# Performance work log

Measured on AMD Instinct MI355X. Metric: run time of the kernel, lower is better.

## Reference

```python
import jax, jax.numpy as jnp
import numpy as np

B, N, H = 2, 1024, 768
MAX_W = 30
WIDTH_D = 20
SPAN_DIM = 3 * H + WIDTH_D  # 2324
K = int(N * 0.4)  # 409 (eval mode: // (1+0) )


def _enumerate_spans(n, max_w):
    # Replicates: enumerate_spans then sorted(spans[::-1], key=start)
    # -> start ascending, end DESCENDING within each start.
    spans = []
    for s in range(n):
        for e in range(min(s + max_w - 1, n - 1), s - 1, -1):
            spans.append((s, e))
    return np.asarray(spans, dtype=np.int32)  # [num_spans, 2]


def setup_inputs() -> dict:
    key = jax.random.key(0)
    ks = jax.random.split(key, 8)
    spans = jnp.asarray(_enumerate_spans(N, MAX_W))  # [30285, 2]
    return {
        "segment_embeddings": jax.random.normal(ks[0], (B, N, H), jnp.float32),
        "segment_mask": jnp.ones((B, N), jnp.int32),
        "candidate_spans": spans,
        "width_emb": jax.random.normal(ks[1], (MAX_W, WIDTH_D), jnp.float32) * 0.02,
        "W1": jax.random.normal(ks[2], (SPAN_DIM, H), jnp.float32) * 0.02,
        "b1": jax.random.normal(ks[3], (H,), jnp.float32) * 0.02,
        "w_s": jax.random.normal(ks[4], (H,), jnp.float32) * 0.02,
        "b_s": jax.random.normal(ks[5], (1,), jnp.float32) * 0.02,
        "k": K,
    }


def reference(segment_embeddings, segment_mask, candidate_spans, width_emb, W1, b1, w_s, b_s, k):
    starts = candidate_spans[:, 0]  # [S]
    ends = candidate_spans[:, 1]    # [S]
    # Endpoint span extractor: x, y, x*y + width embedding (width = end-start)
    x = segment_embeddings[:, starts, :]          # [B,S,H]
    y = segment_embeddings[:, ends, :]            # [B,S,H]
    wemb = width_emb[ends - starts]               # [S,WIDTH_D]
    bsz = segment_embeddings.shape[0]
    span_feat = jnp.concatenate(
        [x, y, x * y, jnp.broadcast_to(wemb[None], (bsz,) + wemb.shape)], axis=-1
    )  # [B,S,3H+WD]
    # MLP (dropout is identity in eval) + GELU (torch default: exact erf)
    h = jax.nn.gelu(jnp.einsum("bsd,dh->bsh", span_feat, W1) + b1, approximate=False)
    scores = jnp.einsum("bsh,h->bs", h, w_s) + b_s[0]  # [B,S]
    # Mask spans whose end index exceeds valid length
    lengths = segment_mask.sum(-1)  # [B]
    scores = scores + jnp.where(ends[None, :] >= lengths[:, None], -1e6, 0.0)
    # Top-k prune, then sort indices and gather
    _, idx = jax.lax.top_k(scores, k)          # [B,k]
    idx = jnp.sort(idx, axis=1)
    top_scores = jnp.take_along_axis(scores, idx, axis=1)            # [B,k]
    top_span_embs = jnp.take_along_axis(h, idx[:, :, None], axis=1)  # [B,k,H]
    top_spans = candidate_spans[idx]                                 # [B,k,2]
    return top_span_embs, top_scores, top_spans
```

## Files before the change

kernel.cpp:

```cpp
#include <hip/hip_runtime.h>
#include <math.h>

#define NB 2
#define NN 1024
#define HH 768
#define MAXW 30
#define KTOP 409
#define BANDCAP 4096
#define BAND_TAU 2e-2f
#define FILTCAP 6144
#define CHT 120
#define GROWS 512

typedef __attribute__((ext_vector_type(4))) float f32x4;
typedef __attribute__((ext_vector_type(8))) __bf16 bf16x8;
typedef __attribute__((ext_vector_type(8))) unsigned short us8;

__device__ __forceinline__ float gelu_f(float z) {
  return 0.5f * z * (1.0f + erff(z * 0.70710678118654752440f));
}
__device__ __forceinline__ unsigned f2key(float f) {
  unsigned u = __float_as_uint(f);
  return (u & 0x80000000u) ? ~u : (u | 0x80000000u);
}
__device__ __forceinline__ float key2f(unsigned k) {
  unsigned u = (k & 0x80000000u) ? (k & 0x7fffffffu) : ~k;
  return __uint_as_float(u);
}
__device__ __forceinline__ unsigned short f2bf_rn(float f) {
  unsigned u = __float_as_uint(f);
  unsigned r = u + 0x7fffu + ((u >> 16) & 1u);
  return (unsigned short)(r >> 16);
}
__device__ __forceinline__ float bf2f(unsigned short h) {
  return __uint_as_float(((unsigned)h) << 16);
}
__device__ __forceinline__ void async_copy16(const void* g, void* l) {
  __builtin_amdgcn_global_load_lds(
      (const __attribute__((address_space(1))) unsigned int*)g,
      (__attribute__((address_space(3))) unsigned int*)l, 16, 0, 0);
}

__global__ void len_kernel(const int* __restrict__ mask, int* __restrict__ lengths) {
  __shared__ int red[256];
  for (int b = 0; b < NB; ++b) {
    int s = 0;
    for (int i = threadIdx.x; i < NN; i += 256) s += mask[b * NN + i];
    red[threadIdx.x] = s;
    __syncthreads();
    for (int off = 128; off > 0; off >>= 1) {
      if (threadIdx.x < off) red[threadIdx.x] += red[threadIdx.x + off];
      __syncthreads();
    }
    if (threadIdx.x == 0) lengths[b] = red[0];
    __syncthreads();
  }
}

__global__ void r_kernel(const float* __restrict__ wemb, const float* __restrict__ W1,
                         const float* __restrict__ b1, float* __restrict__ R) {
  int w = blockIdx.x;
  for (int h = threadIdx.x; h < HH; h += 256) {
    float acc = b1[h];
    for (int j = 0; j < 20; ++j)
      acc = fmaf(wemb[w * 20 + j], W1[(size_t)(3 * HH + j) * HH + h], acc);
    R[w * HH + h] = acc;
  }
}

__global__ __launch_bounds__(256) void prep_bt_kernel(const float* __restrict__ W1,
                                                      unsigned short* __restrict__ Bt,
                                                      unsigned short* __restrict__ Btlo) {
  const int ki = blockIdx.x;
  const int hby = blockIdx.y;
  const float* W1c = W1 + (size_t)(2 * HH) * HH;
  const int t = threadIdx.x;
#pragma unroll
  for (int half = 0; half < 2; ++half) {
    const int c = t + half * 256;
    const int col = c >> 2, kg = c & 3;
    us8 hv, lv;
#pragma unroll
    for (int j = 0; j < 8; ++j) {
      const int k = ki * 32 + kg * 8 + j;
      float v = W1c[(size_t)k * HH + hby * 128 + col];
      unsigned short h = f2bf_rn(v);
      hv[j] = h;
      lv[j] = f2bf_rn(v - bf2f(h));
    }
    const size_t bo = ((size_t)(hby * 24 + ki) * 512 + c) * 8;
    *(us8*)(Bt + bo) = hv;
    *(us8*)(Btlo + bo) = lv;
  }
}

__global__ __launch_bounds__(256) void prep_emb_hl_kernel(
    const float* __restrict__ emb, unsigned short* __restrict__ Ahi,
    unsigned short* __restrict__ Alo) {
  const int tile = blockIdx.x;
  const int ki = blockIdx.y;
  const int t = threadIdx.x;
#pragma unroll
  for (int half = 0; half < 2; ++half) {
    const int c = t + half * 256;
    const int row = c >> 2, kgs = c & 3;
    const int kg = kgs ^ ((row >> 1) & 3);
    const float* xr = emb + (size_t)(tile * 128 + row) * HH;
    const int k0 = ki * 32 + kg * 8;
    float4 x0 = *(const float4*)(xr + k0);
    float4 x1 = *(const float4*)(xr + k0 + 4);
    const float xv[8] = {x0.x, x0.y, x0.z, x0.w, x1.x, x1.y, x1.z, x1.w};
    us8 hv, lv;
#pragma unroll
    for (int j = 0; j < 8; ++j) {
      unsigned short h = f2bf_rn(xv[j]);
      hv[j] = h;
      lv[j] = f2bf_rn(xv[j] - bf2f(h));
    }
    const size_t base = (((size_t)tile * 24 + ki) * 512 + c) * 8;
    *(us8*)(Ahi + base) = hv;
    *(us8*)(Alo + base) = lv;
  }
}

__global__ __launch_bounds__(256) void prep_w1ab_kernel(
    const float* __restrict__ W1, unsigned short* __restrict__ Bhi,
    unsigned short* __restrict__ Blo) {
  const int ki = blockIdx.x;
  const int hby = blockIdx.y;
  const int t = threadIdx.x;
#pragma unroll
  for (int half = 0; half < 2; ++half) {
    const int c = t + half * 256;
    const int col = c >> 2, kg = c & 3;
    const int gc = hby * 128 + col;
    const float* base = W1 + (gc < 768 ? (size_t)0 : (size_t)HH * HH);
    const int n = (gc < 768) ? gc : gc - 768;
    us8 hv, lv;
#pragma unroll
    for (int j = 0; j < 8; ++j) {
      const int k = ki * 32 + kg * 8 + j;
      float v = base[(size_t)k * HH + n];
      unsigned short h = f2bf_rn(v);
      hv[j] = h;
      lv[j] = f2bf_rn(v - bf2f(h));
    }
    const size_t bo = (((size_t)hby * 24 + ki) * 512 + c) * 8;
    *(us8*)(Bhi + bo) = hv;
    *(us8*)(Blo + bo) = lv;
  }
}

__global__ __launch_bounds__(256) void pq_mfma_kernel(
    const unsigned short* __restrict__ Ahi, const unsigned short* __restrict__ Alo,
    const unsigned short* __restrict__ Bhi, const unsigned short* __restrict__ Blo,
    float* __restrict__ P, float* __restrict__ Q) {
  __shared__ unsigned short AsmH[128 * 32], AsmL[128 * 32];
  const int tile = blockIdx.x;
  const int hby = blockIdx.y;
  const int tid = threadIdx.x;
  const int lane = tid & 63, w = tid >> 6;
  const int wm = w & 1, wn = w >> 1;
  const int lm = lane & 15, lq = lane >> 4;

  f32x4 acc[4][4];
#pragma unroll
  for (int i = 0; i < 4; ++i)
#pragma unroll
    for (int j = 0; j < 4; ++j) acc[i][j] = (f32x4){0.f, 0.f, 0.f, 0.f};

  const unsigned short* AbH = Ahi + (size_t)tile * 24 * 4096;
  const unsigned short* AbL = Alo + (size_t)tile * 24 * 4096;
  const unsigned short* BbH = Bhi + (size_t)hby * 24 * 4096;
  const unsigned short* BbL = Blo + (size_t)hby * 24 * 4096;
  const int a_off = (wm * 64 + lm) * 32 + (lq ^ ((lm >> 1) & 3)) * 8;
  const int b_off = (wn * 64 + lm) * 32 + lq * 8;

  for (int ki = 0; ki < 24; ++ki) {
    async_copy16(AbH + (size_t)ki * 4096 + tid * 8, AsmH + tid * 8);
    async_copy16(AbH + (size_t)ki * 4096 + (tid + 256) * 8, AsmH + (tid + 256) * 8);
    async_copy16(AbL + (size_t)ki * 4096 + tid * 8, AsmL + tid * 8);
    async_copy16(AbL + (size_t)ki * 4096 + (tid + 256) * 8, AsmL + (tid + 256) * 8);
    bf16x8 bh[4], bl[4];
#pragma unroll
    for (int ni = 0; ni < 4; ++ni) {
      bh[ni] = *reinterpret_cast<const bf16x8*>(BbH + (size_t)ki * 4096 + b_off + ni * 512);
      bl[ni] = *reinterpret_cast<const bf16x8*>(BbL + (size_t)ki * 4096 + b_off + ni * 512);
    }
    __syncthreads();
    bf16x8 ah[4], al[4];
#pragma unroll
    for (int mi = 0; mi < 4; ++mi) {
      ah[mi] = *reinterpret_cast<const bf16x8*>(AsmH + a_off + mi * 512);
      al[mi] = *reinterpret_cast<const bf16x8*>(AsmL + a_off + mi * 512);
    }
#pragma unroll
    for (int ni = 0; ni < 4; ++ni)
#pragma unroll
      for (int mi = 0; mi < 4; ++mi) {
        acc[mi][ni] = __builtin_amdgcn_mfma_f32_16x16x32_bf16(ah[mi], bh[ni], acc[mi][ni], 0, 0, 0);
        acc[mi][ni] = __builtin_amdgcn_mfma_f32_16x16x32_bf16(ah[mi], bl[ni], acc[mi][ni], 0, 0, 0);
        acc[mi][ni] = __builtin_amdgcn_mfma_f32_16x16x32_bf16(al[mi], bh[ni], acc[mi][ni], 0, 0, 0);
      }
    __syncthreads();
  }

  float* Obase = (hby < 6) ? P : Q;
  const int cb = ((hby < 6) ? hby : hby - 6) * 128 + wn * 64 + lm;
  const int rowb = tile * 128 + wm * 64 + lq * 4;
#pragma unroll
  for (int mi = 0; mi < 4; ++mi)
#pragma unroll
    for (int ni = 0; ni < 4; ++ni)
#pragma unroll
      for (int r = 0; r < 4; ++r)
        Obase[(size_t)(rowb + mi * 16 + r) * HH + cb + ni * 16] = acc[mi][ni][r];
}

__global__ __launch_bounds__(256) void prep_a_kernel(
    const float* __restrict__ emb, const int* __restrict__ spans,
    unsigned short* __restrict__ At, int S, int tileofs) {
  const int tl = blockIdx.x, b = blockIdx.y;
  const int tile = tileofs + tl;
  const int t = threadIdx.x;
#pragma unroll
  for (int half = 0; half < 2; ++half) {
    const int c = t + half * 256;
    const int row = c >> 2, kgs = c & 3;
    const int kg = kgs ^ ((row >> 1) & 3);
    int g = tile * 128 + row;
    if (g >= S) g = S - 1;
    const int s = spans[2 * g], e = spans[2 * g + 1];
    const float* xr = emb + ((size_t)b * NN + s) * HH;
    const float* yr = emb + ((size_t)b * NN + e) * HH;
    unsigned short* dst = At + (((size_t)b * CHT + tl) * 24 * 512 + c) * 8;
    for (int ki = 0; ki < 24; ++ki) {
      const int k0 = ki * 32 + kg * 8;
      float4 x0 = *(const float4*)(xr + k0);
      float4 x1 = *(const float4*)(xr + k0 + 4);
      float4 y0 = *(const float4*)(yr + k0);
      float4 y1 = *(const float4*)(yr + k0 + 4);
      us8 v;
      v[0] = f2bf_rn(x0.x * y0.x); v[1] = f2bf_rn(x0.y * y0.y);
      v[2] = f2bf_rn(x0.z * y0.z); v[3] = f2bf_rn(x0.w * y0.w);
      v[4] = f2bf_rn(x1.x * y1.x); v[5] = f2bf_rn(x1.y * y1.y);
      v[6] = f2bf_rn(x1.z * y1.z); v[7] = f2bf_rn(x1.w * y1.w);
      *(us8*)(dst + (size_t)ki * 4096) = v;
    }
  }
}

__global__ __launch_bounds__(256, 3) void score_mfma3_kernel(
    const int* __restrict__ spans,
    const unsigned short* __restrict__ At, const unsigned short* __restrict__ Bt,
    const float* __restrict__ w_s,
    const float* __restrict__ P, const float* __restrict__ Q, const float* __restrict__ R,
    float* __restrict__ spart, int S, int tileofs) {
  __shared__ unsigned short Asm[128 * 32];
  __shared__ int ssm[128], eem[128], wwm[128];
  __shared__ float sred[128 * 2];

  const int hby = blockIdx.x;
  const int tl = blockIdx.y;
  const int tile = tileofs + tl;
  const int b = blockIdx.z;
  const int tid = threadIdx.x;
  const int lane = tid & 63, w = tid >> 6;
  const int wm = w & 1, wn = w >> 1;
  const int lm = lane & 15, lq = lane >> 4;

  if (tid < 128) {
    int g = tile * 128 + tid;
    int gg = g < S ? g : S - 1;
    int s = spans[2 * gg], e = spans[2 * gg + 1];
    ssm[tid] = s; eem[tid] = e; wwm[tid] = e - s;
  }

  f32x4 acc[4][4];
#pragma unroll
  for (int i = 0; i < 4; ++i)
#pragma unroll
    for (int j = 0; j < 4; ++j) acc[i][j] = (f32x4){0.f, 0.f, 0.f, 0.f};

  const unsigned short* Ab = At + ((size_t)b * CHT + tl) * 24 * 4096;
  const unsigned short* Bb = Bt + (size_t)hby * 24 * 4096;
  const int a_off = (wm * 64 + lm) * 32 + (lq ^ ((lm >> 1) & 3)) * 8;
  const int b_off = (wn * 64 + lm) * 32 + lq * 8;

  for (int ki = 0; ki < 24; ++ki) {
    async_copy16(Ab + (size_t)ki * 4096 + tid * 8, Asm + tid * 8);
    async_copy16(Ab + (size_t)ki * 4096 + (tid + 256) * 8, Asm + (tid + 256) * 8);
    bf16x8 bfr[4];
#pragma unroll
    for (int ni = 0; ni < 4; ++ni)
      bfr[ni] = *reinterpret_cast<const bf16x8*>(Bb + (size_t)ki * 4096 + b_off + ni * 512);
    __syncthreads();
    bf16x8 afr[4];
#pragma unroll
    for (int mi = 0; mi < 4; ++mi)
      afr[mi] = *reinterpret_cast<const bf16x8*>(Asm + a_off + mi * 512);
#pragma unroll
    for (int ni = 0; ni < 4; ++ni)
#pragma unroll
      for (int mi = 0; mi < 4; ++mi)
        acc[mi][ni] = __builtin_amdgcn_mfma_f32_16x16x32_bf16(afr[mi], bfr[ni], acc[mi][ni], 0, 0, 0);
    __syncthreads();
  }

  const int hbg = hby * 128;
  float wsv[4];
#pragma unroll
  for (int ni = 0; ni < 4; ++ni) wsv[ni] = w_s[hbg + wn * 64 + ni * 16 + lm];

#pragma unroll
  for (int mi = 0; mi < 4; ++mi) {
#pragma unroll
    for (int r = 0; r < 4; ++r) {
      const int rowl = wm * 64 + mi * 16 + lq * 4 + r;
      const int s = ssm[rowl], e = eem[rowl], wd = wwm[rowl];
      const float* Pp = P + ((size_t)b * NN + s) * HH + hbg + wn * 64 + lm;
      const float* Qp = Q + ((size_t)b * NN + e) * HH + hbg + wn * 64 + lm;
      const float* Rp = R + (size_t)wd * HH + hbg + wn * 64 + lm;
      float psum = 0.f;
#pragma unroll
      for (int ni = 0; ni < 4; ++ni) {
        float z = acc[mi][ni][r] + Pp[ni * 16] + Qp[ni * 16] + Rp[ni * 16];
        psum = fmaf(gelu_f(z), wsv[ni], psum);
      }
      psum += __shfl_xor(psum, 1);
      psum += __shfl_xor(psum, 2);
      psum += __shfl_xor(psum, 4);
      psum += __shfl_xor(psum, 8);
      if (lm == 0) sred[rowl * 2 + wn] = psum;
    }
  }
  __syncthreads();
  if (tid < 128) {
    int g = tile * 128 + tid;
    if (g < S)
      spart[(size_t)hby * ((size_t)NB * S) + (size_t)b * S + g] = sred[tid * 2] + sred[tid * 2 + 1];
  }
}

__global__ void combine_kernel(const float* __restrict__ sp, const int* __restrict__ spans,
                               const float* __restrict__ b_s, const int* __restrict__ lengths,
                               float* __restrict__ scores, int S) {
  int idx = blockIdx.x * 256 + threadIdx.x;
  if (idx >= NB * S) return;
  int b = idx / S, i = idx - b * S;
  size_t st = (size_t)NB * S;
  float v = b_s[0];
#pragma unroll
  for (int j = 0; j < 6; ++j) v += sp[j * st + idx];
  if (spans[2 * i + 1] >= lengths[b]) v += -1000000.0f;
  scores[idx] = v;
}

__global__ void zero_kernel(unsigned* __restrict__ hist, int* __restrict__ bandcount,
                            int* __restrict__ filtcount) {
  int i = blockIdx.x * 256 + threadIdx.x;
  hist[i] = 0;
  if (blockIdx.x == 0 && threadIdx.x < NB) {
    bandcount[threadIdx.x] = 0;
    filtcount[threadIdx.x] = 0;
  }
}

__global__ void hist16_kernel(const float* __restrict__ scores, unsigned* __restrict__ hist,
                              int S) {
  int idx = blockIdx.x * 256 + threadIdx.x;
  if (idx >= NB * S) return;
  int b = idx / S;
  unsigned key = f2key(scores[idx]) >> 16;
  atomicAdd(&hist[(size_t)b * 65536 + key], 1u);
}

__global__ __launch_bounds__(1024) void scan16_kernel(const unsigned* __restrict__ hist,
                                                      const int* __restrict__ kptr,
                                                      float* __restrict__ pivotf) {
  const int b = blockIdx.x;
  const unsigned* hb = hist + (size_t)b * 65536;
  const int tid = threadIdx.x;
  const unsigned k = (unsigned)kptr[0];
  __shared__ unsigned acc[1024];
  unsigned s = 0;
  for (int j = 0; j < 64; ++j) s += hb[tid * 64 + j];
  const unsigned mysum = s;
  acc[tid] = s;
  __syncthreads();
  for (int off = 1; off < 1024; off <<= 1) {
    unsigned v = (tid + off < 1024) ? acc[tid + off] : 0u;
    __syncthreads();
    acc[tid] += v;
    __syncthreads();
  }
  const unsigned above = acc[tid] - mysum;
  if (above < k && acc[tid] >= k) {
    unsigned cum = above;
    int binf = tid * 64;
    for (int j = 63; j >= 0; --j) {
      unsigned c = hb[tid * 64 + j];
      if (cum + c >= k) { binf = tid * 64 + j; break; }
      cum += c;
    }
    pivotf[b] = key2f(((unsigned)binf) << 16);
  }
}

__global__ void band_kernel(const float* __restrict__ scores, const float* __restrict__ pivotf,
                            int* __restrict__ bandcount, int* __restrict__ bandlist, int S) {
  int idx = blockIdx.x * 256 + threadIdx.x;
  if (idx >= NB * S) return;
  int b = idx / S, i = idx - b * S;
  if (fabsf(scores[idx] - pivotf[b]) <= BAND_TAU) {
    int slot = atomicAdd(&bandcount[b], 1);
    if (slot < BANDCAP) bandlist[b * BANDCAP + slot] = i;
  }
}

__global__ __launch_bounds__(256) void rescore_kernel(
    const float* __restrict__ emb, const int* __restrict__ spans,
    const float* __restrict__ W1, const float* __restrict__ w_s,
    const float* __restrict__ b_s, const int* __restrict__ lengths,
    const float* __restrict__ P, const float* __restrict__ Q, const float* __restrict__ R,
    const int* __restrict__ bandcount, const int* __restrict__ bandlist,
    float* __restrict__ scores, int S) {
  const int b = blockIdx.y;
  int cnt = bandcount[b];
  if (cnt > BANDCAP) cnt = BANDCAP;
  if ((int)blockIdx.x >= cnt) return;
  const int i = bandlist[b * BANDCAP + blockIdx.x];
  const int s = spans[2 * i], e = spans[2 * i + 1], wd = e - s;
  const int tid = threadIdx.x;
  __shared__ float prod[HH];
  __shared__ float red[256];
  for (int c = tid; c < HH; c += 256)
    prod[c] = emb[((size_t)b * NN + s) * HH + c] * emb[((size_t)b * NN + e) * HH + c];
  __syncthreads();
  const float* W1c = W1 + (size_t)(2 * HH) * HH;
  float psum = 0.f;
  for (int c0 = 0; c0 < HH; c0 += 256) {
    const int c = c0 + tid;
    float a = P[((size_t)b * NN + s) * HH + c] + Q[((size_t)b * NN + e) * HH + c] + R[(size_t)wd * HH + c];
    for (int k = 0; k < HH; ++k) a = fmaf(prod[k], W1c[(size_t)k * HH + c], a);
    psum = fmaf(gelu_f(a), w_s[c], psum);
  }
  red[tid] = psum;
  __syncthreads();
  for (int off = 128; off > 0; off >>= 1) {
    if (tid < off) red[tid] += red[tid + off];
    __syncthreads();
  }
  if (tid == 0) {
    float v = red[0] + b_s[0];
    if (e >= lengths[b]) v += -1000000.0f;
    scores[(size_t)b * S + i] = v;
  }
}

__global__ void filt_kernel(const float* __restrict__ scores, const float* __restrict__ pivotf,
                            int* __restrict__ filtcount, int* __restrict__ filtlist, int S) {
  int idx = blockIdx.x * 256 + threadIdx.x;
  if (idx >= NB * S) return;
  int b = idx / S, i = idx - b * S;
  if (scores[idx] > pivotf[b] - 0.01f) {
    int slot = atomicAdd(&filtcount[b], 1);
    if (slot < FILTCAP) filtlist[b * FILTCAP + slot] = i;
  }
}

__global__ __launch_bounds__(1024) void sel_kernel(
    const float* __restrict__ scores, const int* __restrict__ spans,
    const int* __restrict__ kptr, const int* __restrict__ filtcount,
    const int* __restrict__ filtlist,
    float* __restrict__ out_spans, int* __restrict__ sel, int S) {
  const int b = blockIdx.x;
  const int tid = threadIdx.x;
  const int k = kptr[0];
  __shared__ unsigned keys[FILTCAP];
  __shared__ int idxs[FILTCAP];
  __shared__ unsigned hist[256];
  __shared__ unsigned sh_prefix;
  __shared__ int sh_remaining;
  __shared__ int selcnt;
  __shared__ int slist[512];

  int M = filtcount[b];
  if (M > FILTCAP) M = FILTCAP;
  for (int i = tid; i < M; i += 1024) {
    int gi = filtlist[b * FILTCAP + i];
    idxs[i] = gi;
    keys[i] = f2key(scores[(size_t)b * S + gi]);
  }
  if (tid == 0) selcnt = 0;
  __syncthreads();

  unsigned prefix = 0;
  int remaining = k;
  for (int round = 0; round < 4; ++round) {
    const int shift = 24 - 8 * round;
    if (tid < 256) hist[tid] = 0;
    __syncthreads();
    for (int i = tid; i < M; i += 1024) {
      unsigned key = keys[i];
      if (round == 0 || (key >> (shift + 8)) == prefix)
        atomicAdd(&hist[(key >> shift) & 255u], 1u);
    }
    __syncthreads();
    if (tid == 0) {
      int cum = 0;
      for (int bin = 255; bin >= 0; --bin) {
        int c = (int)hist[bin];
        if (cum + c >= remaining) {
          sh_prefix = (prefix << 8) | (unsigned)bin;
          sh_remaining = remaining - cum;
          break;
        }
        cum += c;
      }
    }
    __syncthreads();
    prefix = sh_prefix;
    remaining = sh_remaining;
    __syncthreads();
  }
  const unsigned pk = prefix;
  const int m_eq = remaining;

  for (int i = tid; i < M; i += 1024) {
    unsigned key = keys[i];
    bool pick = false;
    if (key > pk) {
      pick = true;
    } else if (key == pk) {
      int r = 0;
      const int myidx = idxs[i];
      for (int j = 0; j < M; ++j)
        if (keys[j] == pk && idxs[j] < myidx) ++r;
      pick = (r < m_eq);
    }
    if (pick) {
      int p = atomicAdd(&selcnt, 1);
      if (p < 512) slist[p] = idxs[i];
    }
  }
  __syncthreads();

  for (int i = tid; i < k; i += 1024) {
    const int my = slist[i];
    int r = 0;
    for (int j = 0; j < k; ++j) r += (slist[j] < my);
    sel[b * KTOP + r] = my;
    out_spans[(b * KTOP + r) * 2 + 0] = (float)spans[2 * my];
    out_spans[(b * KTOP + r) * 2 + 1] = (float)spans[2 * my + 1];
  }
}

__global__ __launch_bounds__(256) void prep_ga_kernel(
    const float* __restrict__ emb, const int* __restrict__ spans,
    const int* __restrict__ sel, unsigned short* __restrict__ GAhi,
    unsigned short* __restrict__ GAlo) {
  const int bx = blockIdx.x;
  const int tile = bx / 24, ki = bx - tile * 24;
  const int b = blockIdx.y;
  const int t = threadIdx.x;
#pragma unroll
  for (int half = 0; half < 2; ++half) {
    const int c = t + half * 256;
    const int row = c >> 2, kgs = c & 3;
    const int kg = kgs ^ ((row >> 1) & 3);
    int j = tile * 128 + row;
    if (j >= KTOP) j = KTOP - 1;
    const int i = sel[b * KTOP + j];
    const int s = spans[2 * i], e = spans[2 * i + 1];
    const float* xr = emb + ((size_t)b * NN + s) * HH;
    const float* yr = emb + ((size_t)b * NN + e) * HH;
    const int k0 = ki * 32 + kg * 8;
    float4 x0 = *(const float4*)(xr + k0);
    float4 x1 = *(const float4*)(xr + k0 + 4);
    float4 y0 = *(const float4*)(yr + k0);
    float4 y1 = *(const float4*)(yr + k0 + 4);
    const float pv[8] = {x0.x * y0.x, x0.y * y0.y, x0.z * y0.z, x0.w * y0.w,
                         x1.x * y1.x, x1.y * y1.y, x1.z * y1.z, x1.w * y1.w};
    us8 hv, lv;
#pragma unroll
    for (int q = 0; q < 8; ++q) {
      unsigned short h = f2bf_rn(pv[q]);
      hv[q] = h;
      lv[q] = f2bf_rn(pv[q] - bf2f(h));
    }
    const size_t base = (((size_t)(b * 4 + tile) * 24 + ki) * 512 + c) * 8;
    *(us8*)(GAhi + base) = hv;
    *(us8*)(GAlo + base) = lv;
  }
}

__global__ __launch_bounds__(256) void gather_mfma_kernel(
    const int* __restrict__ spans, const int* __restrict__ sel,
    const unsigned short* __restrict__ GAhi, const unsigned short* __restrict__ GAlo,
    const unsigned short* __restrict__ Bt, const unsigned short* __restrict__ Btlo,
    const float* __restrict__ w_s,
    const float* __restrict__ P, const float* __restrict__ Q, const float* __restrict__ R,
    float* __restrict__ outh, float* __restrict__ spartg) {
  __shared__ unsigned short AsmH[128 * 32], AsmL[128 * 32];
  __shared__ int ssm[128], eem[128], wwm[128], vvm[128];
  __shared__ float sred[128 * 2];
  const int tile = blockIdx.x;
  const int hby = blockIdx.y;
  const int b = blockIdx.z;
  const int tid = threadIdx.x;
  const int lane = tid & 63, w = tid >> 6;
  const int wm = w & 1, wn = w >> 1;
  const int lm = lane & 15, lq = lane >> 4;

  if (tid < 128) {
    int j = tile * 128 + tid;
    int valid = (j < KTOP) ? 1 : 0;
    int jj = valid ? j : KTOP - 1;
    int i = sel[b * KTOP + jj];
    ssm[tid] = spans[2 * i];
    eem[tid] = spans[2 * i + 1];
    wwm[tid] = eem[tid] - ssm[tid];
    vvm[tid] = valid;
  }

  f32x4 acc[4][4];
#pragma unroll
  for (int i = 0; i < 4; ++i)
#pragma unroll
    for (int j = 0; j < 4; ++j) acc[i][j] = (f32x4){0.f, 0.f, 0.f, 0.f};

  const unsigned short* AbH = GAhi + (size_t)(b * 4 + tile) * 24 * 4096;
  const unsigned short* AbL = GAlo + (size_t)(b * 4 + tile) * 24 * 4096;
  const unsigned short* BbH = Bt + (size_t)hby * 24 * 4096;
  const unsigned short* BbL = Btlo + (size_t)hby * 24 * 4096;
  const int a_off = (wm * 64 + lm) * 32 + (lq ^ ((lm >> 1) & 3)) * 8;
  const int b_off = (wn * 64 + lm) * 32 + lq * 8;

  for (int ki = 0; ki < 24; ++ki) {
    async_copy16(AbH + (size_t)ki * 4096 + tid * 8, AsmH + tid * 8);
    async_copy16(AbH + (size_t)ki * 4096 + (tid + 256) * 8, AsmH + (tid + 256) * 8);
    async_copy16(AbL + (size_t)ki * 4096 + tid * 8, AsmL + tid * 8);
    async_copy16(AbL + (size_t)ki * 4096 + (tid + 256) * 8, AsmL + (tid + 256) * 8);
    bf16x8 bh[4], bl[4];
#pragma unroll
    for (int ni = 0; ni < 4; ++ni) {
      bh[ni] = *reinterpret_cast<const bf16x8*>(BbH + (size_t)ki * 4096 + b_off + ni * 512);
      bl[ni] = *reinterpret_cast<const bf16x8*>(BbL + (size_t)ki * 4096 + b_off + ni * 512);
    }
    __syncthreads();
    bf16x8 ah[4], al[4];
#pragma unroll
    for (int mi = 0; mi < 4; ++mi) {
      ah[mi] = *reinterpret_cast<const bf16x8*>(AsmH + a_off + mi * 512);
      al[mi] = *reinterpret_cast<const bf16x8*>(AsmL + a_off + mi * 512);
    }
#pragma unroll
    for (int ni = 0; ni < 4; ++ni)
#pragma unroll
      for (int mi = 0; mi < 4; ++mi) {
        acc[mi][ni] = __builtin_amdgcn_mfma_f32_16x16x32_bf16(ah[mi], bh[ni], acc[mi][ni], 0, 0, 0);
        acc[mi][ni] = __builtin_amdgcn_mfma_f32_16x16x32_bf16(ah[mi], bl[ni], acc[mi][ni], 0, 0, 0);
        acc[mi][ni] = __builtin_amdgcn_mfma_f32_16x16x32_bf16(al[mi], bh[ni], acc[mi][ni], 0, 0, 0);
      }
    __syncthreads();
  }

  const int hbg = hby * 128;
  float wsv[4];
#pragma unroll
  for (int ni = 0; ni < 4; ++ni) wsv[ni] = w_s[hbg + wn * 64 + ni * 16 + lm];

#pragma unroll
  for (int mi = 0; mi < 4; ++mi) {
#pragma unroll
    for (int r = 0; r < 4; ++r) {
      const int rowl = wm * 64 + mi * 16 + lq * 4 + r;
      const int s = ssm[rowl], e = eem[rowl], wd = wwm[rowl];
      const float* Pp = P + ((size_t)b * NN + s) * HH + hbg + wn * 64 + lm;
      const float* Qp = Q + ((size_t)b * NN + e) * HH + hbg + wn * 64 + lm;
      const float* Rp = R + (size_t)wd * HH + hbg + wn * 64 + lm;
      float psum = 0.f;
      const int j = tile * 128 + rowl;
      float* op = outh + (size_t)(b * KTOP + j) * HH + hbg + wn * 64 + lm;
#pragma unroll
      for (int ni = 0; ni < 4; ++ni) {
        float z = acc[mi][ni][r] + Pp[ni * 16] + Qp[ni * 16] + Rp[ni * 16];
        float gl = gelu_f(z);
        if (vvm[rowl]) op[ni * 16] = gl;
        psum = fmaf(gl, wsv[ni], psum);
      }
      psum += __shfl_xor(psum, 1);
      psum += __shfl_xor(psum, 2);
      psum += __shfl_xor(psum, 4);
      psum += __shfl_xor(psum, 8);
      if (lm == 0) sred[rowl * 2 + wn] = psum;
    }
  }
  __syncthreads();
  if (tid < 128)
    spartg[(size_t)hby * (NB * GROWS) + b * GROWS + tile * 128 + tid] =
        sred[tid * 2] + sred[tid * 2 + 1];
}

__global__ void score_fin_kernel(const float* __restrict__ spartg, const int* __restrict__ sel,
                                 const int* __restrict__ spans, const float* __restrict__ b_s,
                                 const int* __restrict__ lengths, float* __restrict__ out_scores) {
  int idx = blockIdx.x * 256 + threadIdx.x;
  if (idx >= NB * KTOP) return;
  int b = idx / KTOP, j = idx - b * KTOP;
  float v = b_s[0];
#pragma unroll
  for (int hby = 0; hby < 6; ++hby)
    v += spartg[(size_t)hby * (NB * GROWS) + b * GROWS + j];
  int i = sel[idx];
  if (spans[2 * i + 1] >= lengths[b]) v += -1000000.0f;
  out_scores[idx] = v;
}

extern "C" void kernel_launch(void* const* d_in, const int* in_sizes, int n_in,
                              void* d_out, int out_size, void* d_ws, size_t ws_size,
                              hipStream_t stream) {
  const float* emb = (const float*)d_in[0];
  const int* mask = (const int*)d_in[1];
  const int* spans = (const int*)d_in[2];
  const float* wemb = (const float*)d_in[3];
  const float* W1 = (const float*)d_in[4];
  const float* b1 = (const float*)d_in[5];
  const float* w_s = (const float*)d_in[6];
  const float* b_s = (const float*)d_in[7];
  const int* kptr = (const int*)d_in[8];
  const int S = in_sizes[2] / 2;
  float* out = (float*)d_out;

  char* wp = (char*)d_ws;
  auto take = [&](size_t bytes) {
    char* p = wp;
    wp += (bytes + 63) & ~(size_t)63;
    return p;
  };
  float* Pb = (float*)take((size_t)NB * NN * HH * 4);
  float* Qb = (float*)take((size_t)NB * NN * HH * 4);
  float* Rb = (float*)take((size_t)MAXW * HH * 4);
  float* spart = (float*)take(6 * (size_t)NB * S * 4);
  float* scoresb = (float*)take((size_t)NB * S * 4);
  float* spartg = (float*)take(6 * (size_t)NB * GROWS * 4);
  float* pivotf = (float*)take(NB * 4);
  unsigned short* At = (unsigned short*)take((size_t)NB * CHT * 24 * 4096 * 2);
  unsigned short* Bt = (unsigned short*)take((size_t)6 * 24 * 4096 * 2);
  unsigned short* Btlo = (unsigned short*)take((size_t)6 * 24 * 4096 * 2);
  unsigned short* GAhi = (unsigned short*)take((size_t)NB * 4 * 24 * 4096 * 2);
  unsigned short* GAlo = (unsigned short*)take((size_t)NB * 4 * 24 * 4096 * 2);
  unsigned* hist16b = (unsigned*)take((size_t)NB * 65536 * 4);
  int* selb = (int*)take(NB * KTOP * 4);
  int* lengthsb = (int*)take(NB * 4);
  int* bandcount = (int*)take(NB * 4);
  int* bandlist = (int*)take((size_t)NB * BANDCAP * 4);
  int* filtcount = (int*)take(NB * 4);
  int* filtlist = (int*)take((size_t)NB * FILTCAP * 4);

  unsigned short* AimgHi = At;
  unsigned short* AimgLo = AimgHi + (size_t)16 * 24 * 4096;
  unsigned short* BimgHi = AimgLo + (size_t)16 * 24 * 4096;
  unsigned short* BimgLo = BimgHi + (size_t)12 * 24 * 4096;

  const size_t OFF1 = (size_t)NB * KTOP * HH;
  const size_t OFF2 = OFF1 + (size_t)NB * KTOP;

  const int tiles = (S + 127) / 128;

  len_kernel<<<dim3(1), dim3(256), 0, stream>>>(mask, lengthsb);
  r_kernel<<<dim3(MAXW), dim3(256), 0, stream>>>(wemb, W1, b1, Rb);
  prep_bt_kernel<<<dim3(24, 6), dim3(256), 0, stream>>>(W1, Bt, Btlo);
  prep_emb_hl_kernel<<<dim3(16, 24), dim3(256), 0, stream>>>(emb, AimgHi, AimgLo);
  prep_w1ab_kernel<<<dim3(24, 12), dim3(256), 0, stream>>>(W1, BimgHi, BimgLo);
  pq_mfma_kernel<<<dim3(16, 12), dim3(256), 0, stream>>>(AimgHi, AimgLo, BimgHi, BimgLo, Pb, Qb);
  zero_kernel<<<dim3(512), dim3(256), 0, stream>>>(hist16b, bandcount, filtcount);

  for (int pass = 0; pass < 2; ++pass) {
    const int ofs = pass * CHT;
    const int nt = (pass == 0) ? CHT : (tiles - CHT);
    prep_a_kernel<<<dim3(nt, NB), dim3(256), 0, stream>>>(emb, spans, At, S, ofs);
    score_mfma3_kernel<<<dim3(6, nt, NB), dim3(256), 0, stream>>>(
        spans, At, Bt, w_s, Pb, Qb, Rb, spart, S, ofs);
  }

  combine_kernel<<<dim3((NB * S + 255) / 256), dim3(256), 0, stream>>>(
      spart, spans, b_s, lengthsb, scoresb, S);
  hist16_kernel<<<dim3((NB * S + 255) / 256), dim3(256), 0, stream>>>(scoresb, hist16b, S);
  scan16_kernel<<<dim3(NB), dim3(1024), 0, stream>>>(hist16b, kptr, pivotf);
  band_kernel<<<dim3((NB * S + 255) / 256), dim3(256), 0, stream>>>(
      scoresb, pivotf, bandcount, bandlist, S);
  rescore_kernel<<<dim3(BANDCAP, NB), dim3(256), 0, stream>>>(
      emb, spans, W1, w_s, b_s, lengthsb, Pb, Qb, Rb, bandcount, bandlist, scoresb, S);
  filt_kernel<<<dim3((NB * S + 255) / 256), dim3(256), 0, stream>>>(
      scoresb, pivotf, filtcount, filtlist, S);
  sel_kernel<<<dim3(NB), dim3(1024), 0, stream>>>(
      scoresb, spans, kptr, filtcount, filtlist, out + OFF2, selb, S);
  prep_ga_kernel<<<dim3(96, NB), dim3(256), 0, stream>>>(emb, spans, selb, GAhi, GAlo);
  gather_mfma_kernel<<<dim3(4, 6, NB), dim3(256), 0, stream>>>(
      spans, selb, GAhi, GAlo, Bt, Btlo, w_s, Pb, Qb, Rb, out, spartg);
  score_fin_kernel<<<dim3((NB * KTOP + 255) / 256), dim3(256), 0, stream>>>(
      spartg, selb, spans, b_s, lengthsb, out + OFF1);
}
```

Measured before the change: 581.6 us.

## Fuse x*y bf16 A-tile prep into scoring GEMM with 512-thread blocks

Drops the separate prep_a pass that wrote the x*y bf16 A image to global memory. The scoring kernel now gathers x and y rows directly, multiplies them, converts to bf16 and stores into LDS each k-step. Blocks grow to 512 threads covering 256 output columns, so each A tile is rebuilt only 3 times instead of being read by 6 column blocks, and the two-pass launch loop becomes a single launch. In exchange the A build now sits on the GEMM critical path with an extra barrier per k-step and no async prefetch, and B fragments are loaded per ni inside the loop.

```diff
diff --git a/kernel.cpp b/kernel.cpp
--- a/kernel.cpp
+++ b/kernel.cpp
@@ -9,7 +9,6 @@
 #define BANDCAP 4096
 #define BAND_TAU 2e-2f
 #define FILTCAP 6144
-#define CHT 120
 #define GROWS 512
 
 typedef __attribute__((ext_vector_type(4))) float f32x4;
@@ -217,52 +216,17 @@
         Obase[(size_t)(rowb + mi * 16 + r) * HH + cb + ni * 16] = acc[mi][ni][r];
 }
 
-__global__ __launch_bounds__(256) void prep_a_kernel(
+__global__ __launch_bounds__(512, 4) void score_mfma6_kernel(
     const float* __restrict__ emb, const int* __restrict__ spans,
-    unsigned short* __restrict__ At, int S, int tileofs) {
-  const int tl = blockIdx.x, b = blockIdx.y;
-  const int tile = tileofs + tl;
-  const int t = threadIdx.x;
-#pragma unroll
-  for (int half = 0; half < 2; ++half) {
-    const int c = t + half * 256;
-    const int row = c >> 2, kgs = c & 3;
-    const int kg = kgs ^ ((row >> 1) & 3);
-    int g = tile * 128 + row;
-    if (g >= S) g = S - 1;
-    const int s = spans[2 * g], e = spans[2 * g + 1];
-    const float* xr = emb + ((size_t)b * NN + s) * HH;
-    const float* yr = emb + ((size_t)b * NN + e) * HH;
-    unsigned short* dst = At + (((size_t)b * CHT + tl) * 24 * 512 + c) * 8;
-    for (int ki = 0; ki < 24; ++ki) {
-      const int k0 = ki * 32 + kg * 8;
-      float4 x0 = *(const float4*)(xr + k0);
-      float4 x1 = *(const float4*)(xr + k0 + 4);
-      float4 y0 = *(const float4*)(yr + k0);
-      float4 y1 = *(const float4*)(yr + k0 + 4);
-      us8 v;
-      v[0] = f2bf_rn(x0.x * y0.x); v[1] = f2bf_rn(x0.y * y0.y);
-      v[2] = f2bf_rn(x0.z * y0.z); v[3] = f2bf_rn(x0.w * y0.w);
-      v[4] = f2bf_rn(x1.x * y1.x); v[5] = f2bf_rn(x1.y * y1.y);
-      v[6] = f2bf_rn(x1.z * y1.z); v[7] = f2bf_rn(x1.w * y1.w);
-      *(us8*)(dst + (size_t)ki * 4096) = v;
-    }
-  }
-}
-
-__global__ __launch_bounds__(256, 3) void score_mfma3_kernel(
-    const int* __restrict__ spans,
-    const unsigned short* __restrict__ At, const unsigned short* __restrict__ Bt,
-    const float* __restrict__ w_s,
+    const unsigned short* __restrict__ Bt, const float* __restrict__ w_s,
     const float* __restrict__ P, const float* __restrict__ Q, const float* __restrict__ R,
-    float* __restrict__ spart, int S, int tileofs) {
+    float* __restrict__ spart, int S) {
   __shared__ unsigned short Asm[128 * 32];
   __shared__ int ssm[128], eem[128], wwm[128];
-  __shared__ float sred[128 * 2];
-
-  const int hby = blockIdx.x;
-  const int tl = blockIdx.y;
-  const int tile = tileofs + tl;
+  __shared__ float sred[128 * 4];
+
+  const int colblk = blockIdx.x;
+  const int tile = blockIdx.y;
   const int b = blockIdx.z;
   const int tid = threadIdx.x;
   const int lane = tid & 63, w = tid >> 6;
@@ -275,6 +239,14 @@
     int s = spans[2 * gg], e = spans[2 * gg + 1];
     ssm[tid] = s; eem[tid] = e; wwm[tid] = e - s;
   }
+  __syncthreads();
+
+  const int arow = tid >> 2;
+  const int kgs = tid & 3;
+  const int kg = kgs ^ ((arow >> 1) & 3);
+  const float* xr = emb + ((size_t)b * NN + ssm[arow]) * HH;
+  const float* yr = emb + ((size_t)b * NN + eem[arow]) * HH;
+  const int aw_off = (arow * 4 + kgs) * 8;
 
   f32x4 acc[4][4];
 #pragma unroll
@@ -282,35 +254,42 @@
 #pragma unroll
     for (int j = 0; j < 4; ++j) acc[i][j] = (f32x4){0.f, 0.f, 0.f, 0.f};
 
-  const unsigned short* Ab = At + ((size_t)b * CHT + tl) * 24 * 4096;
+  const int hby = colblk * 2 + (wn >> 1);
   const unsigned short* Bb = Bt + (size_t)hby * 24 * 4096;
+  const int b_off = ((wn & 1) * 64 + lm) * 32 + lq * 8;
   const int a_off = (wm * 64 + lm) * 32 + (lq ^ ((lm >> 1) & 3)) * 8;
-  const int b_off = (wn * 64 + lm) * 32 + lq * 8;
 
   for (int ki = 0; ki < 24; ++ki) {
-    async_copy16(Ab + (size_t)ki * 4096 + tid * 8, Asm + tid * 8);
-    async_copy16(Ab + (size_t)ki * 4096 + (tid + 256) * 8, Asm + (tid + 256) * 8);
-    bf16x8 bfr[4];
-#pragma unroll
-    for (int ni = 0; ni < 4; ++ni)
-      bfr[ni] = *reinterpret_cast<const bf16x8*>(Bb + (size_t)ki * 4096 + b_off + ni * 512);
+    const int k0 = ki * 32 + kg * 8;
+    float4 x0 = *(const float4*)(xr + k0);
+    float4 x1 = *(const float4*)(xr + k0 + 4);
+    float4 y0 = *(const float4*)(yr + k0);
+    float4 y1 = *(const float4*)(yr + k0 + 4);
+    us8 v;
+    v[0] = f2bf_rn(x0.x * y0.x); v[1] = f2bf_rn(x0.y * y0.y);
+    v[2] = f2bf_rn(x0.z * y0.z); v[3] = f2bf_rn(x0.w * y0.w);
+    v[4] = f2bf_rn(x1.x * y1.x); v[5] = f2bf_rn(x1.y * y1.y);
+    v[6] = f2bf_rn(x1.z * y1.z); v[7] = f2bf_rn(x1.w * y1.w);
+    __syncthreads();
+    *(us8*)(Asm + aw_off) = v;
     __syncthreads();
     bf16x8 afr[4];
 #pragma unroll
     for (int mi = 0; mi < 4; ++mi)
       afr[mi] = *reinterpret_cast<const bf16x8*>(Asm + a_off + mi * 512);
 #pragma unroll
-    for (int ni = 0; ni < 4; ++ni)
+    for (int ni = 0; ni < 4; ++ni) {
+      bf16x8 bfr = *reinterpret_cast<const bf16x8*>(Bb + (size_t)ki * 4096 + b_off + ni * 512);
 #pragma unroll
       for (int mi = 0; mi < 4; ++mi)
-        acc[mi][ni] = __builtin_amdgcn_mfma_f32_16x16x32_bf16(afr[mi], bfr[ni], acc[mi][ni], 0, 0, 0);
-    __syncthreads();
-  }
-
-  const int hbg = hby * 128;
+        acc[mi][ni] = __builtin_amdgcn_mfma_f32_16x16x32_bf16(afr[mi], bfr, acc[mi][ni], 0, 0, 0);
+    }
+  }
+
+  const int cbase = colblk * 256 + wn * 64 + lm;
   float wsv[4];
 #pragma unroll
-  for (int ni = 0; ni < 4; ++ni) wsv[ni] = w_s[hbg + wn * 64 + ni * 16 + lm];
+  for (int ni = 0; ni < 4; ++ni) wsv[ni] = w_s[cbase + ni * 16];
 
 #pragma unroll
   for (int mi = 0; mi < 4; ++mi) {
@@ -318,9 +297,9 @@
     for (int r = 0; r < 4; ++r) {
       const int rowl = wm * 64 + mi * 16 + lq * 4 + r;
       const int s = ssm[rowl], e = eem[rowl], wd = wwm[rowl];
-      const float* Pp = P + ((size_t)b * NN + s) * HH + hbg + wn * 64 + lm;
-      const float* Qp = Q + ((size_t)b * NN + e) * HH + hbg + wn * 64 + lm;
-      const float* Rp = R + (size_t)wd * HH + hbg + wn * 64 + lm;
+      const float* Pp = P + ((size_t)b * NN + s) * HH + cbase;
+      const float* Qp = Q + ((size_t)b * NN + e) * HH + cbase;
+      const float* Rp = R + (size_t)wd * HH + cbase;
       float psum = 0.f;
 #pragma unroll
       for (int ni = 0; ni < 4; ++ni) {
@@ -331,14 +310,15 @@
       psum += __shfl_xor(psum, 2);
       psum += __shfl_xor(psum, 4);
       psum += __shfl_xor(psum, 8);
-      if (lm == 0) sred[rowl * 2 + wn] = psum;
+      if (lm == 0) sred[rowl * 4 + wn] = psum;
     }
   }
   __syncthreads();
   if (tid < 128) {
     int g = tile * 128 + tid;
     if (g < S)
-      spart[(size_t)hby * ((size_t)NB * S) + (size_t)b * S + g] = sred[tid * 2] + sred[tid * 2 + 1];
+      spart[(size_t)colblk * ((size_t)NB * S) + (size_t)b * S + g] =
+          sred[tid * 4] + sred[tid * 4 + 1] + sred[tid * 4 + 2] + sred[tid * 4 + 3];
   }
 }
 
@@ -351,7 +331,7 @@
   size_t st = (size_t)NB * S;
   float v = b_s[0];
 #pragma unroll
-  for (int j = 0; j < 6; ++j) v += sp[j * st + idx];
+  for (int j = 0; j < 3; ++j) v += sp[j * st + idx];
   if (spans[2 * i + 1] >= lengths[b]) v += -1000000.0f;
   scores[idx] = v;
 }
@@ -742,11 +722,14 @@
   float* Pb = (float*)take((size_t)NB * NN * HH * 4);
   float* Qb = (float*)take((size_t)NB * NN * HH * 4);
   float* Rb = (float*)take((size_t)MAXW * HH * 4);
-  float* spart = (float*)take(6 * (size_t)NB * S * 4);
+  float* spart = (float*)take(3 * (size_t)NB * S * 4);
   float* scoresb = (float*)take((size_t)NB * S * 4);
   float* spartg = (float*)take(6 * (size_t)NB * GROWS * 4);
   float* pivotf = (float*)take(NB * 4);
-  unsigned short* At = (unsigned short*)take((size_t)NB * CHT * 24 * 4096 * 2);
+  unsigned short* AimgHi = (unsigned short*)take((size_t)16 * 24 * 4096 * 2);
+  unsigned short* AimgLo = (unsigned short*)take((size_t)16 * 24 * 4096 * 2);
+  unsigned short* BimgHi = (unsigned short*)take((size_t)12 * 24 * 4096 * 2);
+  unsigned short* BimgLo = (unsigned short*)take((size_t)12 * 24 * 4096 * 2);
   unsigned short* Bt = (unsigned short*)take((size_t)6 * 24 * 4096 * 2);
   unsigned short* Btlo = (unsigned short*)take((size_t)6 * 24 * 4096 * 2);
   unsigned short* GAhi = (unsigned short*)take((size_t)NB * 4 * 24 * 4096 * 2);
@@ -759,11 +742,6 @@
   int* filtcount = (int*)take(NB * 4);
   int* filtlist = (int*)take((size_t)NB * FILTCAP * 4);
 
-  unsigned short* AimgHi = At;
-  unsigned short* AimgLo = AimgHi + (size_t)16 * 24 * 4096;
-  unsigned short* BimgHi = AimgLo + (size_t)16 * 24 * 4096;
-  unsigned short* BimgLo = BimgHi + (size_t)12 * 24 * 4096;
-
   const size_t OFF1 = (size_t)NB * KTOP * HH;
   const size_t OFF2 = OFF1 + (size_t)NB * KTOP;
 
@@ -777,13 +755,8 @@
   pq_mfma_kernel<<<dim3(16, 12), dim3(256), 0, stream>>>(AimgHi, AimgLo, BimgHi, BimgLo, Pb, Qb);
   zero_kernel<<<dim3(512), dim3(256), 0, stream>>>(hist16b, bandcount, filtcount);
 
-  for (int pass = 0; pass < 2; ++pass) {
-    const int ofs = pass * CHT;
-    const int nt = (pass == 0) ? CHT : (tiles - CHT);
-    prep_a_kernel<<<dim3(nt, NB), dim3(256), 0, stream>>>(emb, spans, At, S, ofs);
-    score_mfma3_kernel<<<dim3(6, nt, NB), dim3(256), 0, stream>>>(
-        spans, At, Bt, w_s, Pb, Qb, Rb, spart, S, ofs);
-  }
+  score_mfma6_kernel<<<dim3(3, tiles, NB), dim3(512), 0, stream>>>(
+      emb, spans, Bt, w_s, Pb, Qb, Rb, spart, S);
 
   combine_kernel<<<dim3((NB * S + 255) / 256), dim3(256), 0, stream>>>(
       spart, spans, b_s, lengthsb, scoresb, S);
```

Result: faster. 550.0 us (-5.4%).
